# Kernel optimization log

Hardware: AMD Instinct MI355X
Metric: run time of the kernel (lower is better)

Reference implementation:

```python
import jax, jax.numpy as jnp
import numpy as np

V, L, H, D = 2048, 16, 8, 64   # vocab, max_chars, n_head, word_vec_d
B = 8192                        # number of words in batch (rows of char_code)
NW_TOTAL = 8192                 # len(word_code)
N_NAMES = 2048                  # total names (4 words each)
N_GROUPS = 8                    # groups of names (256 each)
PAD = 0
TEMP = D ** 0.5
LN_EPS = 1e-5


def make_pos():
    freq = D // 2
    inv = 1.0 / np.power(10000.0, np.arange(freq) / freq)
    ph = np.outer(np.arange(L), inv)
    return jnp.asarray(np.hstack([np.cos(ph), np.sin(ph)]).astype(np.float32))


def setup_inputs() -> dict:
    key = jax.random.key(0)
    ks = jax.random.split(key, 8)
    char_emb = jax.random.normal(ks[0], (V, D), jnp.float32) * 0.02
    char_emb = char_emb.at[PAD].set(0.0)  # padding_idx row
    Wc = jax.random.normal(ks[1], (D, 3 * H * D), jnp.float32) * 0.02
    bc = jnp.zeros((3 * H * D,), jnp.float32)
    Wp = jax.random.normal(ks[2], (D, 3 * H * D), jnp.float32) * 0.02
    bp = jnp.zeros((3 * H * D,), jnp.float32)
    gamma = jnp.ones((D,), jnp.float32)
    beta = jnp.zeros((D,), jnp.float32)
    W1 = jax.random.normal(ks[3], (H, 16), jnp.float32) * 0.1
    b1 = jnp.zeros((16,), jnp.float32)
    W2 = jax.random.normal(ks[4], (16, 8), jnp.float32) * 0.1
    b2 = jnp.zeros((8,), jnp.float32)
    char_code = jax.random.randint(ks[5], (B, L), 1, V)
    char_code = char_code.at[::4, -2:].set(PAD)  # some padded tails
    word_code = jax.random.randint(ks[6], (NW_TOTAL,), 0, B)
    n_words = np.full((N_NAMES,), NW_TOTAL // N_NAMES, dtype=np.int64)
    n_names = np.full((N_GROUPS,), N_NAMES // N_GROUPS, dtype=np.int64)
    return {"char_emb": char_emb, "Wc": Wc, "bc": bc, "Wp": Wp, "bp": bp,
            "gamma": gamma, "beta": beta, "W1": W1, "b1": b1, "W2": W2, "b2": b2,
            "char_code": char_code, "word_code": word_code,
            "n_words": n_words, "n_names": n_names}


def reference(char_emb, Wc, bc, Wp, bp, gamma, beta, W1, b1, W2, b2,
              char_code, word_code, n_words, n_names):
    pos = make_pos()
    # ComputeQKV: linear d -> 3*H*d, reshape [N,3,H,D]
    cqkv = (char_emb @ Wc + bc).reshape(V, 3, H, D)
    cq, ck, cv = cqkv[:, 0], cqkv[:, 1], cqkv[:, 2]        # [V,H,D]
    pqkv = (pos @ Wp + bp).reshape(L, 3, H, D)
    pq, pk, pv = pqkv[:, 0], pqkv[:, 1], pqkv[:, 2]        # [L,H,D]
    # precomputed score tables
    char_qk = jnp.einsum('xhd,yhd->hxy', cq, ck).at[:, :, PAD].set(-1e9)  # [H,V,V]
    pos_qk = jnp.einsum('xhd,yhd->hxy', pq, pk)                            # [H,L,L]
    # char_q@pos_k + (pos_q@char_k)^T summed over the first dim of char_pos_qk
    cp = jnp.einsum('vhd,lhd->hvl', cq, pk) + jnp.einsum('lhd,vhd->hvl', pq, ck)  # [H,V,L]
    code = char_code                                        # [B,L]
    # gather-assembled scores, no [H,B*L,V] intermediate
    sim = (char_qk[:, code[:, :, None], code[:, None, :]]   # [H,B,L,L]
           + cp[:, code]
           + pos_qk[:, None]) / TEMP
    attn = jax.nn.softmax(sim, axis=-1)                     # [H,B,L,L] (dropout=0)
    v = jnp.transpose(cv[code], (2, 0, 1, 3)) + pv.transpose(1, 0, 2)[:, None]  # [H,B,L,D]
    out = jnp.einsum('hbij,hbjd->bihd', attn, v)            # [B,L,H,D]
    mu = out.mean(-1, keepdims=True)
    var = out.var(-1, keepdims=True)
    out = (out - mu) / jnp.sqrt(var + LN_EPS) * gamma + beta  # LayerNorm(D)
    char_ft = jnp.transpose(out, (0, 2, 1, 3))              # [B,H,L,D]
    mask = (code != PAD)
    pooled = jnp.einsum('bl,bhld->bhd', mask.astype(out.dtype), char_ft) \
             / mask.sum(-1)[:, None, None]                  # masked mean over chars
    x = jnp.transpose(pooled, (0, 2, 1))                    # [B,D,H]
    x = jax.nn.relu(x @ W1 + b1) @ W2 + b2                  # MLP over head dim -> [B,D,8]
    word_ft = x.reshape(B, -1)[word_code]                   # [NW_TOTAL, D*8]
    nw = np.asarray(n_words)
    seg = jnp.asarray(np.repeat(np.arange(nw.size), nw))
    name_ft = jax.ops.segment_sum(word_ft, seg, num_segments=nw.size) \
              / jnp.asarray(nw, word_ft.dtype)[:, None]     # ragged mean -> [N_NAMES, D*8]
    splits = np.cumsum(np.asarray(n_names))[:-1]
    return tuple(jnp.split(name_ft, splits, axis=0))
```

## Files before the change

kernel.cpp:

```cpp
#include <hip/hip_runtime.h>
#include <hip/hip_bf16.h>
#include <math.h>

typedef __attribute__((ext_vector_type(8))) short bfrag;
typedef __attribute__((ext_vector_type(4))) float ffrag;
typedef __attribute__((ext_vector_type(4))) float f4v;
typedef __attribute__((ext_vector_type(2))) float f2v;

#define C3 1536
#define PS 24

__device__ __forceinline__ unsigned short f2bf(float f) {
    unsigned u = __float_as_uint(f);
    return (unsigned short)((u + 0x7FFFu + ((u >> 16) & 1u)) >> 16);
}

__device__ __forceinline__ float row16_sum(float x) {
    int v;
    v = __builtin_amdgcn_update_dpp(0, __float_as_int(x), 0xB1, 0xF, 0xF, true);
    x += __int_as_float(v);
    v = __builtin_amdgcn_update_dpp(0, __float_as_int(x), 0x4E, 0xF, 0xF, true);
    x += __int_as_float(v);
    v = __builtin_amdgcn_update_dpp(0, __float_as_int(x), 0x124, 0xF, 0xF, true);
    x += __int_as_float(v);
    v = __builtin_amdgcn_update_dpp(0, __float_as_int(x), 0x128, 0xF, 0xF, true);
    x += __int_as_float(v);
    return x;
}

__global__ __launch_bounds__(256) void precompute_kernel(
    const float* __restrict__ char_emb, const float* __restrict__ Wc, const float* __restrict__ bc,
    const float* __restrict__ Wp, const float* __restrict__ bp,
    const float* __restrict__ gamma, const float* __restrict__ beta,
    unsigned short* __restrict__ cqkv, unsigned short* __restrict__ pbf,
    unsigned short* __restrict__ pvb, float* __restrict__ gbtab)
{
    const int b = blockIdx.x;
    const int t = threadIdx.x;
    if (b < 1536) {
        const int mt = b / 6;
        const int nt = b - mt * 6;
        const int m0 = mt * 8;
        const int c = nt * 256 + t;
        const float qs = (c < 512) ? 0.125f : 1.f;
        const float bias = bc[c];
        float acc[8];
        #pragma unroll
        for (int r = 0; r < 8; ++r) acc[r] = bias;
        #pragma unroll 16
        for (int dd = 0; dd < 64; ++dd) {
            const float wv = Wc[dd * C3 + c];
            #pragma unroll
            for (int r = 0; r < 8; ++r)
                acc[r] = fmaf(char_emb[(m0 + r) * 64 + dd], wv, acc[r]);
        }
        #pragma unroll
        for (int r = 0; r < 8; ++r)
            cqkv[(size_t)(m0 + r) * C3 + c] = f2bf(acc[r] * qs);
    } else {
        const int e = b - 1536;
        const int l = e / 6;
        const int cc = e - l * 6;
        if (b == 1536 && t < 64) {
            #pragma unroll
            for (int dt = 0; dt < 4; ++dt) {
                gbtab[t * 8 + dt]     = gamma[dt * 16 + t];
                gbtab[t * 8 + 4 + dt] = beta[dt * 16 + t];
            }
        }
        __shared__ float spos[64];
        if (t < 64) {
            const int f = t & 31;
            const float inv = exp2f(-(float)f * 0.41524101186092034f);
            const float ph = (float)l * inv;
            spos[t] = (t < 32) ? cosf(ph) : sinf(ph);
        }
        __syncthreads();
        const int c = t + cc * 256;
        float acc = bp[c];
        #pragma unroll
        for (int dd = 0; dd < 64; ++dd)
            acc = fmaf(spos[dd], Wp[dd * C3 + c], acc);
        if (c < 1024) {
            const float qs = (c < 512) ? 0.125f : 1.f;
            pbf[(c >> 6) * 1024 + l * 64 + (c & 63)] = f2bf(acc * qs);
        } else {
            const int h = (c >> 6) & 7, d = c & 63;
            pvb[((h * 4 + (d >> 4)) * 2 + (l >> 3)) * 128 + (d & 15) * 8 + (l & 7)] = f2bf(acc);
        }
    }
}

__global__ __launch_bounds__(256, 7) void attn_kernel(
    const unsigned short* __restrict__ cqkv, const unsigned short* __restrict__ pbf,
    const unsigned short* __restrict__ pvb, const int* __restrict__ char_code,
    const float* __restrict__ gbtab,
    const float* __restrict__ W1, const float* __restrict__ b1,
    const float* __restrict__ W2, const float* __restrict__ b2,
    float* __restrict__ x)
{
    __shared__ __attribute__((aligned(16))) unsigned short sVt[4 * 1024];
    __shared__ __attribute__((aligned(16))) unsigned short sP[4 * 16 * PS];
    __shared__ float sPool[512];
    __shared__ float sHid[64 * 17];
    __shared__ float sWb[280];

    const int t = threadIdx.x;
    const int lane = t & 63;
    const int wid = t >> 6;
    const int w = blockIdx.x;
    const int quad = lane >> 4;
    const int n = lane & 15;
    const int q2 = quad & 1;

    if (t < 128) { sWb[t] = W1[t]; sWb[144 + t] = W2[t]; }
    else if (t < 144) sWb[t] = b1[t - 128];
    else if (t < 152) sWb[272 + (t - 144)] = b2[t - 144];

    const int code = char_code[w * 16 + n];
    const bool kvalid = (code != 0);
    const unsigned long long msk = __ballot(kvalid);
    const int nv = __popcll(msk & 0xFFFFull);

    const f4v g4 = *(const f4v*)(gbtab + n * 8);
    const f4v b4 = *(const f4v*)(gbtab + n * 8 + 4);

    unsigned short* vt = sVt + wid * 1024;
    unsigned short* pt = sP + wid * 16 * PS;

    bfrag onesf;
    #pragma unroll
    for (int j = 0; j < 8; ++j) onesf[j] = (short)0x3F80;

    #pragma unroll
    for (int c2 = 0; c2 < 2; ++c2) {
        const int h = wid + c2 * 4;

        const unsigned short* cvp = cqkv + (size_t)code * C3 + 1024 + h * 64;
        #pragma unroll
        for (int cc = 0; cc < 2; ++cc) {
            const int d8 = quad + cc * 4;
            const bfrag cv = *(const bfrag*)(cvp + d8 * 8);
            #pragma unroll
            for (int j = 0; j < 8; ++j) {
                const int d = d8 * 8 + j;
                const int e = ((d >> 4) * 2 + (n >> 3)) * 128
                            + ((d & 15) ^ ((n >> 3) << 2)) * 8 + (n & 7);
                vt[e] = (unsigned short)cv[j];
            }
        }

        ffrag accS = {0.f, 0.f, 0.f, 0.f};
        const unsigned short* cbase = cqkv + (size_t)code * C3 + h * 64;
        const unsigned short* pq = pbf + h * 1024 + n * 64;
        const unsigned short* pk = pbf + (8 + h) * 1024 + n * 64;
        #pragma unroll
        for (int cc = 0; cc < 2; ++cc) {
            const int off = quad * 8 + cc * 32;
            const bfrag cqF = *(const bfrag*)(cbase + off);
            const bfrag ckF = *(const bfrag*)(cbase + 512 + off);
            const bfrag pqF = *(const bfrag*)(pq + off);
            const bfrag pkF = *(const bfrag*)(pk + off);
            accS = __builtin_amdgcn_mfma_f32_16x16x32_bf16(cqF, ckF, accS, 0, 0, 0);
            accS = __builtin_amdgcn_mfma_f32_16x16x32_bf16(cqF, pkF, accS, 0, 0, 0);
            accS = __builtin_amdgcn_mfma_f32_16x16x32_bf16(ckF, pqF, accS, 0, 0, 0);
            accS = __builtin_amdgcn_mfma_f32_16x16x32_bf16(pqF, pkF, accS, 0, 0, 0);
        }

        #pragma unroll
        for (int r = 0; r < 4; ++r) {
            const float pr = kvalid ? __expf(accS[r]) : 0.f;
            pt[(quad * 4 + r) * PS + n] = f2bf(pr);
        }

        bfrag ap;
        #pragma unroll
        for (int j = 0; j < 8; ++j) ap[j] = 0;
        if (quad < 2) ap = *(const bfrag*)(pt + n * PS + quad * 8);
        ffrag accO[4];
        #pragma unroll
        for (int dt = 0; dt < 4; ++dt) { ffrag z = {0.f,0.f,0.f,0.f}; accO[dt] = z; }
        #pragma unroll
        for (int dt = 0; dt < 4; ++dt) {
            const bfrag bcv = *(const bfrag*)(vt + (dt * 2 + q2) * 128 + (n ^ (q2 << 2)) * 8);
            accO[dt] = __builtin_amdgcn_mfma_f32_16x16x32_bf16(ap, bcv, accO[dt], 0, 0, 0);
            const bfrag bpv = *(const bfrag*)(pvb + ((h * 4 + dt) * 2 + q2) * 128 + n * 8);
            accO[dt] = __builtin_amdgcn_mfma_f32_16x16x32_bf16(ap, bpv, accO[dt], 0, 0, 0);
        }
        ffrag accE = {0.f, 0.f, 0.f, 0.f};
        accE = __builtin_amdgcn_mfma_f32_16x16x32_bf16(ap, onesf, accE, 0, 0, 0);

        float ps1[4], ps2[4];
        #pragma unroll
        for (int r = 0; r < 4; ++r) {
            ps1[r] = accO[0][r] + accO[1][r] + accO[2][r] + accO[3][r];
            ps2[r] = accO[0][r]*accO[0][r] + accO[1][r]*accO[1][r]
                   + accO[2][r]*accO[2][r] + accO[3][r]*accO[3][r];
            ps1[r] = row16_sum(ps1[r]);
            ps2[r] = row16_sum(ps2[r]);
        }
        float pool[4] = {0.f, 0.f, 0.f, 0.f};
        #pragma unroll
        for (int r = 0; r < 4; ++r) {
            const float mu   = ps1[r] * 0.015625f;
            const float var  = fmaxf(ps2[r] * 0.015625f - mu * mu, 0.f);
            const float rstd = rsqrtf(var + accE[r] * accE[r] * 1e-5f);
            const float iv = ((msk >> (quad * 4 + r)) & 1ull) ? 1.f : 0.f;
            #pragma unroll
            for (int dt = 0; dt < 4; ++dt)
                pool[dt] += iv * fmaf((accO[dt][r] - mu) * rstd, g4[dt], b4[dt]);
        }
        #pragma unroll
        for (int xm = 16; xm <= 32; xm <<= 1) {
            #pragma unroll
            for (int dt = 0; dt < 4; ++dt) pool[dt] += __shfl_xor(pool[dt], xm);
        }
        if (quad == 0) {
            const float invnv = 1.f / (float)nv;
            #pragma unroll
            for (int dt = 0; dt < 4; ++dt)
                sPool[h * 64 + n * 4 + dt] = pool[dt] * invnv;
        }
    }
    __syncthreads();

    if (t < 64) {
        const int dmap = (t & 15) * 4 + (t >> 4);
        float pl[8];
        #pragma unroll
        for (int hh = 0; hh < 8; ++hh) pl[hh] = sPool[hh * 64 + dmap];
        #pragma unroll
        for (int c = 0; c < 16; ++c) {
            float hs = sWb[128 + c];
            #pragma unroll
            for (int hh = 0; hh < 8; ++hh) hs = fmaf(pl[hh], sWb[hh * 16 + c], hs);
            sHid[t * 17 + c] = fmaxf(hs, 0.f);
        }
    }
    __syncthreads();
    {
        const int d = t >> 2, o0 = (t & 3) * 2;
        float a0 = sWb[272 + o0], a1 = sWb[272 + o0 + 1];
        #pragma unroll
        for (int c = 0; c < 16; ++c) {
            const float hc = sHid[d * 17 + c];
            a0 = fmaf(hc, sWb[144 + c * 8 + o0], a0);
            a1 = fmaf(hc, sWb[144 + c * 8 + o0 + 1], a1);
        }
        f2v res; res[0] = a0; res[1] = a1;
        *(f2v*)(x + (size_t)w * 512 + t * 2) = res;
    }
}

__global__ __launch_bounds__(256) void name_avg_kernel(
    const float* __restrict__ x, const int* __restrict__ word_code,
    const int* __restrict__ n_words, float* __restrict__ out)
{
    const int t = threadIdx.x;
    const int lane = t & 63;
    const int nm = blockIdx.x * 4 + (t >> 6);

    int part = 0;
    for (int i = lane; i < nm; i += 64) part += n_words[i];
    #pragma unroll
    for (int xm = 1; xm <= 32; xm <<= 1) part += __shfl_xor(part, xm);
    const int off = part;
    const int cnt = n_words[nm];

    f4v a0 = {0.f,0.f,0.f,0.f}, a1 = {0.f,0.f,0.f,0.f};
    for (int r = 0; r < cnt; ++r) {
        const int wc = word_code[off + r];
        const f4v u0 = *(const f4v*)(x + (size_t)wc * 512 + lane * 8);
        const f4v u1 = *(const f4v*)(x + (size_t)wc * 512 + lane * 8 + 4);
        #pragma unroll
        for (int k = 0; k < 4; ++k) { a0[k] += u0[k]; a1[k] += u1[k]; }
    }
    const float inv = 1.f / (float)cnt;
    #pragma unroll
    for (int k = 0; k < 4; ++k) { a0[k] *= inv; a1[k] *= inv; }
    *(f4v*)(out + (size_t)nm * 512 + lane * 8) = a0;
    *(f4v*)(out + (size_t)nm * 512 + lane * 8 + 4) = a1;
}

extern "C" void kernel_launch(void* const* d_in, const int* in_sizes, int n_in,
                              void* d_out, int out_size, void* d_ws, size_t ws_size,
                              hipStream_t stream) {
    (void)in_sizes; (void)n_in; (void)out_size; (void)ws_size;
    const float* char_emb = (const float*)d_in[0];
    const float* Wc    = (const float*)d_in[1];
    const float* bc    = (const float*)d_in[2];
    const float* Wp    = (const float*)d_in[3];
    const float* bp    = (const float*)d_in[4];
    const float* gamma = (const float*)d_in[5];
    const float* beta  = (const float*)d_in[6];
    const float* W1    = (const float*)d_in[7];
    const float* b1    = (const float*)d_in[8];
    const float* W2    = (const float*)d_in[9];
    const float* b2    = (const float*)d_in[10];
    const int* char_code = (const int*)d_in[11];
    const int* word_code = (const int*)d_in[12];
    const int* n_words   = (const int*)d_in[13];

    char* ws = (char*)d_ws;
    unsigned short* cqkv = (unsigned short*)ws;
    unsigned short* pbf  = (unsigned short*)(ws + 6291456);
    unsigned short* pvb  = (unsigned short*)(ws + 6324224);
    float* x     = (float*)(ws + 6340608);
    float* gbtab = (float*)(ws + 23117824);
    float* out = (float*)d_out;

    precompute_kernel<<<1632, 256, 0, stream>>>(char_emb, Wc, bc, Wp, bp, gamma, beta,
                                                cqkv, pbf, pvb, gbtab);
    attn_kernel<<<8192, 256, 0, stream>>>(cqkv, pbf, pvb, char_code, gbtab,
                                          W1, b1, W2, b2, x);
    name_avg_kernel<<<512, 256, 0, stream>>>(x, word_code, n_words, out);
}
```

Before: 206.9 us.

## Precompute char-position and position-position score tables in a separate kernel

Adds a cp_kernel that precomputes, per vocabulary entry and head, the cross terms q_char·k_pos + k_char·q_pos for every position, plus a shared pos-pos score table. The attention kernel then starts its score accumulator from these tables via gathered loads and keeps only the char-char MFMA, cutting its per-block MFMA work from four products to one. The cost is an extra kernel launch and a tables pass over the vocabulary, plus scattered global gathers in the attention kernel. The occupancy hint drops from 7 to 5 waves.

Result: faster. 199.9 us (-3.4%).

```diff
diff --git a/kernel.cpp b/kernel.cpp
--- a/kernel.cpp
+++ b/kernel.cpp
@@ -13,6 +13,9 @@
 __device__ __forceinline__ unsigned short f2bf(float f) {
     unsigned u = __float_as_uint(f);
     return (unsigned short)((u + 0x7FFFu + ((u >> 16) & 1u)) >> 16);
+}
+__device__ __forceinline__ float bf2f(unsigned short u) {
+    return __uint_as_float((unsigned)u << 16);
 }
 
 __device__ __forceinline__ float row16_sum(float x) {
@@ -91,10 +94,57 @@
     }
 }
 
-__global__ __launch_bounds__(256, 7) void attn_kernel(
+__global__ __launch_bounds__(128) void cp_kernel(
     const unsigned short* __restrict__ cqkv, const unsigned short* __restrict__ pbf,
+    float* __restrict__ cps, float* __restrict__ pqk)
+{
+    const int b = blockIdx.x;
+    const int t = threadIdx.x;
+    if (b < 2048) {
+        const int h = t >> 4, l = t & 15;
+        const unsigned short* cq = cqkv + (size_t)b * C3 + h * 64;
+        const unsigned short* ck = cqkv + (size_t)b * C3 + 512 + h * 64;
+        const unsigned short* pq = pbf + h * 1024 + l * 64;
+        const unsigned short* pk = pbf + (8 + h) * 1024 + l * 64;
+        float s = 0.f;
+        #pragma unroll
+        for (int c8 = 0; c8 < 8; ++c8) {
+            const bfrag a = *(const bfrag*)(cq + c8 * 8);
+            const bfrag bb = *(const bfrag*)(pk + c8 * 8);
+            const bfrag c = *(const bfrag*)(ck + c8 * 8);
+            const bfrag d = *(const bfrag*)(pq + c8 * 8);
+            #pragma unroll
+            for (int j = 0; j < 8; ++j)
+                s += bf2f((unsigned short)a[j]) * bf2f((unsigned short)bb[j])
+                   + bf2f((unsigned short)c[j]) * bf2f((unsigned short)d[j]);
+        }
+        cps[((size_t)h * 2048 + b) * 16 + l] = s;
+    } else {
+        #pragma unroll
+        for (int i = 0; i < 16; ++i) {
+            const int e = t * 16 + i;
+            const int h = e >> 8, r = (e >> 4) & 15, c = e & 15;
+            const unsigned short* pq = pbf + h * 1024 + r * 64;
+            const unsigned short* pk = pbf + (8 + h) * 1024 + c * 64;
+            float s = 0.f;
+            #pragma unroll
+            for (int c8 = 0; c8 < 8; ++c8) {
+                const bfrag a = *(const bfrag*)(pq + c8 * 8);
+                const bfrag bb = *(const bfrag*)(pk + c8 * 8);
+                #pragma unroll
+                for (int j = 0; j < 8; ++j)
+                    s += bf2f((unsigned short)a[j]) * bf2f((unsigned short)bb[j]);
+            }
+            pqk[e] = s;
+        }
+    }
+}
+
+__global__ __launch_bounds__(256, 5) void attn_kernel(
+    const unsigned short* __restrict__ cqkv,
     const unsigned short* __restrict__ pvb, const int* __restrict__ char_code,
     const float* __restrict__ gbtab,
+    const float* __restrict__ cps, const float* __restrict__ pqk,
     const float* __restrict__ W1, const float* __restrict__ b1,
     const float* __restrict__ W2, const float* __restrict__ b2,
     float* __restrict__ x)
@@ -122,6 +172,10 @@
     const unsigned long long msk = __ballot(kvalid);
     const int nv = __popcll(msk & 0xFFFFull);
 
+    int rc[4];
+    #pragma unroll
+    for (int rr = 0; rr < 4; ++rr) rc[rr] = __shfl(code, quad * 4 + rr);
+
     const f4v g4 = *(const f4v*)(gbtab + n * 8);
     const f4v b4 = *(const f4v*)(gbtab + n * 8 + 4);
 
@@ -150,21 +204,19 @@
             }
         }
 
-        ffrag accS = {0.f, 0.f, 0.f, 0.f};
+        const float* cph = cps + (size_t)h * 32768;
+        const float* pqh = pqk + h * 256;
+        ffrag accS;
+        #pragma unroll
+        for (int rr = 0; rr < 4; ++rr)
+            accS[rr] = cph[rc[rr] * 16 + n] + pqh[(quad * 4 + rr) * 16 + n];
         const unsigned short* cbase = cqkv + (size_t)code * C3 + h * 64;
-        const unsigned short* pq = pbf + h * 1024 + n * 64;
-        const unsigned short* pk = pbf + (8 + h) * 1024 + n * 64;
         #pragma unroll
         for (int cc = 0; cc < 2; ++cc) {
             const int off = quad * 8 + cc * 32;
             const bfrag cqF = *(const bfrag*)(cbase + off);
             const bfrag ckF = *(const bfrag*)(cbase + 512 + off);
-            const bfrag pqF = *(const bfrag*)(pq + off);
-            const bfrag pkF = *(const bfrag*)(pk + off);
             accS = __builtin_amdgcn_mfma_f32_16x16x32_bf16(cqF, ckF, accS, 0, 0, 0);
-            accS = __builtin_amdgcn_mfma_f32_16x16x32_bf16(cqF, pkF, accS, 0, 0, 0);
-            accS = __builtin_amdgcn_mfma_f32_16x16x32_bf16(ckF, pqF, accS, 0, 0, 0);
-            accS = __builtin_amdgcn_mfma_f32_16x16x32_bf16(pqF, pkF, accS, 0, 0, 0);
         }
 
         #pragma unroll
@@ -307,11 +359,14 @@
     unsigned short* pvb  = (unsigned short*)(ws + 6324224);
     float* x     = (float*)(ws + 6340608);
     float* gbtab = (float*)(ws + 23117824);
+    float* cps   = (float*)(ws + 23119872);
+    float* pqk   = (float*)(ws + 24168448);
     float* out = (float*)d_out;
 
     precompute_kernel<<<1632, 256, 0, stream>>>(char_emb, Wc, bc, Wp, bp, gamma, beta,
                                                 cqkv, pbf, pvb, gbtab);
-    attn_kernel<<<8192, 256, 0, stream>>>(cqkv, pbf, pvb, char_code, gbtab,
+    cp_kernel<<<2049, 128, 0, stream>>>(cqkv, pbf, cps, pqk);
+    attn_kernel<<<8192, 256, 0, stream>>>(cqkv, pvb, char_code, gbtab, cps, pqk,
                                           W1, b1, W2, b2, x);
     name_avg_kernel<<<512, 256, 0, stream>>>(x, word_code, n_words, out);
 }
```
